# Performance work log

Measured on AMD Instinct MI355X. Metric: run time of the kernel, lower is better.

## Reference

```python
import jax, jax.numpy as jnp
import numpy as np

V = 1_000_000   # variables
F = 4_200_000   # functions (clauses), ratio ~4.2
K = 3           # literals per clause
E = K * F       # edges
T = 5           # fixed number of peel iterations (peel update is idempotent once converged)


def setup_inputs() -> dict:
    key = jax.random.key(0)
    k1, k2 = jax.random.split(key, 2)
    vidx = jax.random.randint(k1, (E,), 0, V, dtype=jnp.int32)
    fidx = jnp.repeat(jnp.arange(F, dtype=jnp.int32), K)  # each clause touches K variables
    graph_map = jnp.stack([vidx, fidx])  # [2, E]
    edge_feature = (2 * jax.random.randint(k2, (E,), 0, 2) - 1).astype(jnp.float32)  # +/-1 literal signs
    active_variables = jnp.ones((V, 1), jnp.float32)
    active_functions = jnp.ones((F, 1), jnp.float32)
    return dict(graph_map=graph_map, edge_feature=edge_feature,
                active_variables=active_variables, active_functions=active_functions)


def reference(graph_map, edge_feature, active_variables, active_functions):
    """Peeling propagation over the bipartite variable-function graph.

    Equivalent to the torch sparse-mm formulation:
      vf_map @ x        == segment_sum(x[fidx], vidx, V)
      signed_vf_map @ x == segment_sum(edge_feature * x[fidx], vidx, V)
      vf_map^T @ y      == segment_sum(y[vidx], fidx, F)
    """
    nV = active_variables.shape[0]
    nF = active_functions.shape[0]
    vidx = graph_map[0]
    fidx = graph_map[1]
    ef = edge_feature[:, None]  # [E,1]

    def seg_v(x_f):        # vf_map @ x_f : [F,1] -> [V,1]
        return jax.ops.segment_sum(x_f[fidx], vidx, num_segments=nV)

    def seg_v_signed(x_f):  # signed_vf_map @ x_f
        return jax.ops.segment_sum(ef * x_f[fidx], vidx, num_segments=nV)

    def seg_f(x_v):        # vf_map^T @ x_v : [V,1] -> [F,1]
        return jax.ops.segment_sum(x_v[vidx], fidx, num_segments=nF)

    variable_degree = seg_v(active_functions)
    signed_variable_degree = seg_v_signed(active_functions)

    def step(carry, _):
        av, af, deg, sdeg = carry
        # variables whose active clause occurrences all share one sign
        single_v = (deg == jnp.abs(sdeg)).astype(deg.dtype) * av
        # active clauses touched by those variables become satisfied
        single_f = (seg_f(single_v) > 0).astype(af.dtype) * af
        deg = deg - seg_v(single_f) * av
        sdeg = sdeg - seg_v_signed(single_f) * av
        av = av * (1.0 - single_v)
        af = af * (1.0 - single_f)
        return (av, af, deg, sdeg), None

    (av, af, deg, sdeg), _ = jax.lax.scan(
        step, (active_variables, active_functions, variable_degree, signed_variable_degree),
        None, length=T)
    return deg  # residual variable degrees after peeling [V,1]
```

## Files before the change

kernel.cpp:

```cpp
#include <hip/hip_runtime.h>


static constexpr int Vn = 1000000;
static constexpr int Fn = 4200000;
static constexpr int Tn = 5;

static constexpr int SBLK = 2048;
static constexpr int FPB  = 2052;
static constexpr int BIN_BITS = 10;
static constexpr int BIN_SIZE = 1 << BIN_BITS;
static constexpr int NB  = (Vn + BIN_SIZE - 1) >> BIN_BITS;
static constexpr int NBP = 1024;
static constexpr int CH_BITS = 12;
static constexpr int CH_SIZE = 1 << CH_BITS;
static constexpr int NCH = (Vn + CH_SIZE - 1) >> CH_BITS;
static constexpr int RCAP = 3 * FPB;
static constexpr int RSTRIDE = (RCAP + 63) & ~63;
static constexpr int OROW = 1024;
static constexpr int AVW = NCH * (CH_SIZE / 64);

__global__ __launch_bounds__(256) void k_pack_sort(
    const int* __restrict__ vidx, const float* __restrict__ ef,
    const float* __restrict__ afunc,
    unsigned long long* __restrict__ gpack,
    unsigned short* __restrict__ offs,
    unsigned short* __restrict__ sorted,
    unsigned int* __restrict__ tmp,
    unsigned char* __restrict__ tgrp)
{
    __shared__ unsigned int hist[NBP];
    __shared__ unsigned int cur[NBP];
    __shared__ unsigned int wsum[4];
    __shared__ unsigned int s_total;
    __shared__ __align__(16) unsigned short st[RSTRIDE];

    const int k = blockIdx.x;
    const int f0 = k * FPB;
    int n = Fn - f0; if (n < 0) n = 0; if (n > FPB) n = FPB;
    const int n4 = n >> 2;

    for (int i = threadIdx.x; i < NBP; i += 256) hist[i] = 0u;
    __syncthreads();

    for (int j = threadIdx.x; j < n4; j += 256) {
        const int fb = f0 + 4 * j, e = 3 * fb;
        int4 va = *(const int4*)(vidx + e);
        int4 vb = *(const int4*)(vidx + e + 4);
        int4 vc = *(const int4*)(vidx + e + 8);
        float4 ea = *(const float4*)(ef + e);
        float4 eb = *(const float4*)(ef + e + 4);
        float4 ec = *(const float4*)(ef + e + 8);
        float4 a4 = *(const float4*)(afunc + fb);
        int      vv[12] = {va.x, va.y, va.z, va.w, vb.x, vb.y, vb.z, vb.w, vc.x, vc.y, vc.z, vc.w};
        float    ss[12] = {ea.x, ea.y, ea.z, ea.w, eb.x, eb.y, eb.z, eb.w, ec.x, ec.y, ec.z, ec.w};
        float    aa[4]  = {a4.x, a4.y, a4.z, a4.w};
        unsigned long long gq[4];
        #pragma unroll
        for (int q = 0; q < 4; ++q) {
            int v0 = vv[3 * q], v1 = vv[3 * q + 1], v2 = vv[3 * q + 2];
            unsigned int s0 = ss[3 * q]     > 0.0f ? 1u : 0u;
            unsigned int s1 = ss[3 * q + 1] > 0.0f ? 1u : 0u;
            unsigned int s2 = ss[3 * q + 2] > 0.0f ? 1u : 0u;
            unsigned int act = aa[q] != 0.0f ? 1u : 0u;
            gq[q] = (unsigned long long)(unsigned int)v0
                  | ((unsigned long long)(unsigned int)v1 << 20)
                  | ((unsigned long long)(unsigned int)v2 << 40)
                  | ((unsigned long long)s0 << 60)
                  | ((unsigned long long)s1 << 61)
                  | ((unsigned long long)s2 << 62)
                  | ((unsigned long long)act << 63);
            if (act) {
                atomicAdd(&hist[v0 >> BIN_BITS], 1u);
                atomicAdd(&hist[v1 >> BIN_BITS], 1u);
                atomicAdd(&hist[v2 >> BIN_BITS], 1u);
            }
        }
        *(ulonglong2*)(gpack + fb)     = make_ulonglong2(gq[0], gq[1]);
        *(ulonglong2*)(gpack + fb + 2) = make_ulonglong2(gq[2], gq[3]);
    }
    for (int i = 4 * n4 + threadIdx.x; i < n; i += 256) {
        const int f = f0 + i, e0 = 3 * f;
        int v0 = vidx[e0], v1 = vidx[e0 + 1], v2 = vidx[e0 + 2];
        unsigned int s0 = ef[e0]     > 0.0f ? 1u : 0u;
        unsigned int s1 = ef[e0 + 1] > 0.0f ? 1u : 0u;
        unsigned int s2 = ef[e0 + 2] > 0.0f ? 1u : 0u;
        unsigned int act = afunc[f] != 0.0f ? 1u : 0u;
        unsigned long long g = (unsigned long long)(unsigned int)v0
                             | ((unsigned long long)(unsigned int)v1 << 20)
                             | ((unsigned long long)(unsigned int)v2 << 40)
                             | ((unsigned long long)s0 << 60)
                             | ((unsigned long long)s1 << 61)
                             | ((unsigned long long)s2 << 62)
                             | ((unsigned long long)act << 63);
        gpack[f] = g;
        if (act) {
            atomicAdd(&hist[v0 >> BIN_BITS], 1u);
            atomicAdd(&hist[v1 >> BIN_BITS], 1u);
            atomicAdd(&hist[v2 >> BIN_BITS], 1u);
        }
    }
    __syncthreads();

    {
        const int t = threadIdx.x, lane = t & 63, wid = t >> 6;
        unsigned int a0 = hist[4 * t], a1 = hist[4 * t + 1];
        unsigned int a2 = hist[4 * t + 2], a3 = hist[4 * t + 3];
        unsigned int tsum = a0 + a1 + a2 + a3;
        unsigned int x = tsum;
        #pragma unroll
        for (int off = 1; off < 64; off <<= 1) {
            unsigned int y = (unsigned int)__shfl_up((int)x, off);
            if (lane >= off) x += y;
        }
        if (lane == 63) wsum[wid] = x;
        __syncthreads();
        unsigned int wbase = 0;
        for (int w = 0; w < wid; ++w) wbase += wsum[w];
        unsigned int e0x = wbase + x - tsum;
        unsigned int e1x = e0x + a0, e2x = e1x + a1, e3x = e2x + a2;
        cur[4 * t] = e0x; cur[4 * t + 1] = e1x; cur[4 * t + 2] = e2x; cur[4 * t + 3] = e3x;
        if (t == 255) s_total = e3x + a3;
        unsigned short* row = offs + (size_t)k * OROW;
        if (4 * t     <= NB) row[4 * t]     = (unsigned short)e0x;
        if (4 * t + 1 <= NB) row[4 * t + 1] = (unsigned short)e1x;
        if (4 * t + 2 <= NB) row[4 * t + 2] = (unsigned short)e2x;
        if (4 * t + 3 <= NB) row[4 * t + 3] = (unsigned short)e3x;
    }
    __syncthreads();

    for (int j = threadIdx.x; j < n4; j += 256) {
        const int fb = f0 + 4 * j;
        ulonglong2 ga = *(const ulonglong2*)(gpack + fb);
        ulonglong2 gb = *(const ulonglong2*)(gpack + fb + 2);
        unsigned long long gq[4] = {ga.x, ga.y, gb.x, gb.y};
        #pragma unroll
        for (int q = 0; q < 4; ++q) {
            unsigned long long g = gq[q];
            if ((long long)g < 0) {
                unsigned int v0 = (unsigned int)(g & 0xFFFFFu);
                unsigned int v1 = (unsigned int)((g >> 20) & 0xFFFFFu);
                unsigned int v2 = (unsigned int)((g >> 40) & 0xFFFFFu);
                unsigned int sl0 = atomicAdd(&cur[v0 >> BIN_BITS], 1u);
                st[sl0] = (unsigned short)((v0 & (CH_SIZE - 1)) | ((unsigned int)((g >> 60) & 1u) << CH_BITS));
                unsigned int sl1 = atomicAdd(&cur[v1 >> BIN_BITS], 1u);
                st[sl1] = (unsigned short)((v1 & (CH_SIZE - 1)) | ((unsigned int)((g >> 61) & 1u) << CH_BITS));
                unsigned int sl2 = atomicAdd(&cur[v2 >> BIN_BITS], 1u);
                st[sl2] = (unsigned short)((v2 & (CH_SIZE - 1)) | ((unsigned int)((g >> 62) & 1u) << CH_BITS));
            }
        }
    }
    for (int i = 4 * n4 + threadIdx.x; i < n; i += 256) {
        unsigned long long g = gpack[f0 + i];
        if ((long long)g < 0) {
            unsigned int v0 = (unsigned int)(g & 0xFFFFFu);
            unsigned int v1 = (unsigned int)((g >> 20) & 0xFFFFFu);
            unsigned int v2 = (unsigned int)((g >> 40) & 0xFFFFFu);
            unsigned int sl0 = atomicAdd(&cur[v0 >> BIN_BITS], 1u);
            st[sl0] = (unsigned short)((v0 & (CH_SIZE - 1)) | ((unsigned int)((g >> 60) & 1u) << CH_BITS));
            unsigned int sl1 = atomicAdd(&cur[v1 >> BIN_BITS], 1u);
            st[sl1] = (unsigned short)((v1 & (CH_SIZE - 1)) | ((unsigned int)((g >> 61) & 1u) << CH_BITS));
            unsigned int sl2 = atomicAdd(&cur[v2 >> BIN_BITS], 1u);
            st[sl2] = (unsigned short)((v2 & (CH_SIZE - 1)) | ((unsigned int)((g >> 62) & 1u) << CH_BITS));
        }
    }
    __syncthreads();

    {
        const int tot = (int)s_total;
        const int nvec = (tot + 7) >> 3;
        int4* __restrict__ dst = (int4*)(sorted + (size_t)k * RSTRIDE);
        const int4* __restrict__ src = (const int4*)st;
        for (int i = threadIdx.x; i < nvec; i += 256) dst[i] = src[i];
    }

    {
        const int gt = blockIdx.x * 256 + threadIdx.x;
        const int gs = SBLK * 256;
        for (int i = gt; i < Vn; i += gs) tmp[i] = 0u;
        for (int i = gt; i < AVW; i += gs) tgrp[i] = 0;
    }
}

__global__ __launch_bounds__(256) void k_transpose(const unsigned short* __restrict__ in,
                                                   unsigned short* __restrict__ out) {
    __shared__ unsigned short t[64][65];
    const int bx = blockIdx.x;
    const int by = blockIdx.y;
    for (int i = threadIdx.x; i < 64 * 64; i += 256) {
        int r = i >> 6, c = i & 63;
        t[r][c] = in[(size_t)(by * 64 + r) * OROW + (bx * 64 + c)];
    }
    __syncthreads();
    for (int i = threadIdx.x; i < 64 * 64; i += 256) {
        int r = i >> 6, c = i & 63;
        out[(size_t)(bx * 64 + r) * SBLK + (by * 64 + c)] = t[c][r];
    }
}

__device__ __forceinline__ unsigned char subdirty8(unsigned long long m) {
    unsigned char b = 0;
    #pragma unroll
    for (int j = 0; j < 8; ++j) b |= (unsigned char)((((m >> (8 * j)) & 0xFFull) ? 1u : 0u) << j);
    return b;
}

__global__ __launch_bounds__(1024) void k_accum(
    const unsigned short* __restrict__ offs_T,
    const unsigned short* __restrict__ sorted,
    const float* __restrict__ avars,
    unsigned int* __restrict__ packed,
    unsigned long long* __restrict__ avm,
    unsigned long long* __restrict__ svm,
    unsigned char* __restrict__ sgrp8)
{
    __shared__ unsigned int acc[CH_SIZE];
    __shared__ unsigned short row0[SBLK];
    __shared__ unsigned short row1[SBLK];
    const int c = blockIdx.x;
    const int r0 = 4 * c;
    const int r1 = (4 * c + 4 < NB) ? (4 * c + 4) : NB;
    for (int i = threadIdx.x; i < CH_SIZE; i += 1024) acc[i] = 0u;
    for (int i = threadIdx.x; i < SBLK; i += 1024) {
        row0[i] = offs_T[(size_t)r0 * SBLK + i];
        row1[i] = offs_T[(size_t)r1 * SBLK + i];
    }
    __syncthreads();
    for (int k = threadIdx.x; k < SBLK; k += 1024) {
        const int s0 = row0[k], s1 = row1[k];
        const unsigned short* seg = sorted + (size_t)k * RSTRIDE;
        int e = s0;
        for (; e < s1 && (e & 3); ++e) {
            unsigned int p = seg[e];
            atomicAdd(&acc[p & (CH_SIZE - 1)], 0x10000u | (p >> CH_BITS));
        }
        for (; e + 4 <= s1; e += 4) {
            unsigned long long q = *(const unsigned long long*)(seg + e);
            #pragma unroll
            for (int j = 0; j < 4; ++j) {
                unsigned int p = (unsigned int)((q >> (16 * j)) & 0xFFFFu);
                atomicAdd(&acc[p & (CH_SIZE - 1)], 0x10000u | (p >> CH_BITS));
            }
        }
        for (; e < s1; ++e) {
            unsigned int p = seg[e];
            atomicAdd(&acc[p & (CH_SIZE - 1)], 0x10000u | (p >> CH_BITS));
        }
    }
    __syncthreads();
    const int vbase = c << CH_BITS;
    for (int i = threadIdx.x; i < CH_SIZE; i += 1024) {
        int v = vbase + i;
        bool valid = v < Vn;
        unsigned int p = valid ? acc[i] : 0u;
        bool av = valid && (avars[v] != 0.0f);
        unsigned int cnt = p >> 16, pos = p & 0xFFFFu;
        bool sv = av && (pos == 0u || pos == cnt);
        unsigned long long avb = __ballot(av);
        unsigned long long svb = __ballot(sv);
        if (valid) packed[v] = p;
        if ((threadIdx.x & 63) == 0) {
            avm[v >> 6] = avb;
            svm[v >> 6] = svb;
            sgrp8[v >> 6] = subdirty8(svb);
        }
    }
}

__device__ __forceinline__ void fire_one(unsigned long long g, int f,
                                         unsigned long long* __restrict__ gpack,
                                         const unsigned int* __restrict__ svm32,
                                         const unsigned char* __restrict__ s8,
                                         unsigned int* __restrict__ tmp,
                                         unsigned char* __restrict__ tgrp)
{
    if ((long long)g >= 0) return;
    unsigned int v0 = (unsigned int)(g & 0xFFFFFu);
    unsigned int v1 = (unsigned int)((g >> 20) & 0xFFFFFu);
    unsigned int v2 = (unsigned int)((g >> 40) & 0xFFFFFu);
    unsigned int h0 = (unsigned int)(s8[v0 >> 6] >> ((v0 >> 3) & 7u)) & 1u;
    unsigned int h1 = (unsigned int)(s8[v1 >> 6] >> ((v1 >> 3) & 7u)) & 1u;
    unsigned int h2 = (unsigned int)(s8[v2 >> 6] >> ((v2 >> 3) & 7u)) & 1u;
    if (!(h0 | h1 | h2)) return;
    unsigned int hit = ((svm32[v0 >> 5] >> (v0 & 31u)) |
                        (svm32[v1 >> 5] >> (v1 & 31u)) |
                        (svm32[v2 >> 5] >> (v2 & 31u))) & 1u;
    if (!hit) return;
    gpack[f] = g & ~(1ull << 63);
    atomicAdd(&tmp[v0], 0x10000u | (unsigned int)((g >> 60) & 1u));
    atomicAdd(&tmp[v1], 0x10000u | (unsigned int)((g >> 61) & 1u));
    atomicAdd(&tmp[v2], 0x10000u | (unsigned int)((g >> 62) & 1u));
    tgrp[v0 >> 6] = 1; tgrp[v1 >> 6] = 1; tgrp[v2 >> 6] = 1;
}

__global__ __launch_bounds__(256) void k_funcs(unsigned long long* __restrict__ gpack,
                        const unsigned int* __restrict__ svm32,
                        const unsigned char* __restrict__ sgrp8,
                        unsigned int* __restrict__ tmp,
                        unsigned char* __restrict__ tgrp)
{
    __shared__ __align__(16) unsigned char s8[AVW];
    for (int i = threadIdx.x; i < AVW / 16; i += 256)
        ((int4*)s8)[i] = ((const int4*)sgrp8)[i];
    __syncthreads();
    const int gid = blockIdx.x * 256 + threadIdx.x;
    const int f = 8 * gid;
    if (f >= Fn) return;
    ulonglong2 ga = *(const ulonglong2*)(gpack + f);
    ulonglong2 gb = *(const ulonglong2*)(gpack + f + 2);
    ulonglong2 gc = *(const ulonglong2*)(gpack + f + 4);
    ulonglong2 gd = *(const ulonglong2*)(gpack + f + 6);
    fire_one(ga.x, f,     gpack, svm32, s8, tmp, tgrp);
    fire_one(ga.y, f + 1, gpack, svm32, s8, tmp, tgrp);
    fire_one(gb.x, f + 2, gpack, svm32, s8, tmp, tgrp);
    fire_one(gb.y, f + 3, gpack, svm32, s8, tmp, tgrp);
    fire_one(gc.x, f + 4, gpack, svm32, s8, tmp, tgrp);
    fire_one(gc.y, f + 5, gpack, svm32, s8, tmp, tgrp);
    fire_one(gd.x, f + 6, gpack, svm32, s8, tmp, tgrp);
    fire_one(gd.y, f + 7, gpack, svm32, s8, tmp, tgrp);
}

__global__ void k_update(unsigned int* __restrict__ packed,
                         unsigned int* __restrict__ tmp,
                         unsigned long long* __restrict__ avm,
                         unsigned long long* __restrict__ svm,
                         unsigned char* __restrict__ sgrp8,
                         unsigned char* __restrict__ tgrp,
                         float* __restrict__ deg, int write_deg)
{
    const int v = blockIdx.x * blockDim.x + threadIdx.x;
    const int lane = threadIdx.x & 63;
    const bool valid = v < Vn;
    unsigned long long avw = 0ull, svw = 0ull;
    unsigned char tg = 0;
    if (valid) {
        avw = avm[v >> 6]; svw = svm[v >> 6];
        tg = tgrp[v >> 6];
    }
    if (!write_deg && !tg && svw == 0ull) return;
    const bool av_old = valid && ((avw >> lane) & 1ull);
    const bool sv     = valid && ((svw >> lane) & 1ull);
    const bool av_new = av_old && !sv;
    unsigned int p = 0u;
    if (valid) {
        p = packed[v];
        if (tg) {
            unsigned int tp = tmp[v];
            if (tp != 0u) {
                if (av_old) { p -= tp; packed[v] = p; }
                tmp[v] = 0u;
            }
        }
    }
    const unsigned int c = p >> 16, pos = p & 0xFFFFu;
    const bool nsv = av_new && (pos == 0u || pos == c);
    unsigned long long nsvb = __ballot(nsv);
    if (lane == 0 && valid) {
        svm[v >> 6] = nsvb;
        avm[v >> 6] = avw & ~svw;
        sgrp8[v >> 6] = subdirty8(nsvb);
        if (tg) tgrp[v >> 6] = 0;
    }
    if (write_deg && valid) deg[v] = (float)c;
}

extern "C" void kernel_launch(void* const* d_in, const int* in_sizes, int n_in,
                              void* d_out, int out_size, void* d_ws, size_t ws_size,
                              hipStream_t stream) {
    const int*   graph_map        = (const int*)d_in[0];
    const float* edge_feature     = (const float*)d_in[1];
    const float* active_variables = (const float*)d_in[2];
    const float* active_functions = (const float*)d_in[3];
    const int* vidx = graph_map;

    float* deg = (float*)d_out;
    char* ws = (char*)d_ws;
    size_t off = 0;
    auto alloc = [&](size_t bytes) -> void* {
        void* p = ws + off; off += (bytes + 255) & ~(size_t)255; return p;
    };
    unsigned long long* gpack = (unsigned long long*)alloc(8ull * Fn);
    unsigned int* packed      = (unsigned int*)alloc(4ull * Vn);
    unsigned long long* avm   = (unsigned long long*)alloc(8ull * AVW);
    unsigned long long* svm   = (unsigned long long*)alloc(8ull * AVW);
    unsigned char* sgrp8      = (unsigned char*)alloc(AVW);
    unsigned char* tgrp       = (unsigned char*)alloc(AVW);
    unsigned short* offs      = (unsigned short*)alloc(2ull * SBLK * OROW);
    unsigned short* offs_T    = (unsigned short*)alloc(2ull * SBLK * OROW);
    unsigned short* sorted    = (unsigned short*)alloc(2ull * SBLK * RSTRIDE);
    unsigned int* tmp         = (unsigned int*)alloc(4ull * Vn);

    const int BS = 256;
    const int gV = (Vn + BS - 1) / BS;
    const int gF8 = (Fn / 8 + BS - 1) / BS;

    k_pack_sort<<<SBLK, 256, 0, stream>>>(vidx, edge_feature, active_functions,
                                          gpack, offs, sorted, tmp, tgrp);
    k_transpose<<<dim3(OROW / 64, SBLK / 64), 256, 0, stream>>>(offs, offs_T);
    k_accum<<<NCH, 1024, 0, stream>>>(offs_T, sorted, active_variables, packed, avm, svm, sgrp8);
    for (int t = 0; t < Tn; ++t) {
        k_funcs<<<gF8, BS, 0, stream>>>(gpack, (const unsigned int*)svm, sgrp8, tmp, tgrp);
        k_update<<<gV, BS, 0, stream>>>(packed, tmp, avm, svm, sgrp8, tgrp, deg, (t == Tn - 1) ? 1 : 0);
    }
}
```

Baseline: 312.3 us.

## Replace binned sort-based degree accumulation with direct global atomics and persistent funcs grid

Drops the per-block histogram/counting-sort, offset transpose and chunked shared-memory accumulation kernels. Degrees and signed counts are now accumulated with global atomicAdd directly into the packed per-variable word during packing, followed by a simple decode kernel. A separate zeroing kernel is added, and k_funcs becomes a grid-stride loop over a fixed 1024 blocks so the per-block shared sgrp8 load is amortized. This trades the sort's locality for about 12.6M scattered global atomics onto 1M addresses.

```diff
diff --git a/kernel.cpp b/kernel.cpp
--- a/kernel.cpp
+++ b/kernel.cpp
@@ -5,196 +5,66 @@
 static constexpr int Fn = 4200000;
 static constexpr int Tn = 5;
 
-static constexpr int SBLK = 2048;
-static constexpr int FPB  = 2052;
-static constexpr int BIN_BITS = 10;
-static constexpr int BIN_SIZE = 1 << BIN_BITS;
-static constexpr int NB  = (Vn + BIN_SIZE - 1) >> BIN_BITS;
-static constexpr int NBP = 1024;
-static constexpr int CH_BITS = 12;
-static constexpr int CH_SIZE = 1 << CH_BITS;
-static constexpr int NCH = (Vn + CH_SIZE - 1) >> CH_BITS;
-static constexpr int RCAP = 3 * FPB;
-static constexpr int RSTRIDE = (RCAP + 63) & ~63;
-static constexpr int OROW = 1024;
+static constexpr int CH_SIZE = 4096;
+static constexpr int NCH = (Vn + CH_SIZE - 1) / CH_SIZE;
 static constexpr int AVW = NCH * (CH_SIZE / 64);
 
-__global__ __launch_bounds__(256) void k_pack_sort(
+__global__ __launch_bounds__(256) void k_zero(unsigned int* __restrict__ packed,
+                                              unsigned int* __restrict__ tmp,
+                                              unsigned char* __restrict__ tgrp)
+{
+    const int i = blockIdx.x * 256 + threadIdx.x;
+    const int4 z = make_int4(0, 0, 0, 0);
+    if (i < Vn / 4) {
+        ((int4*)packed)[i] = z;
+        ((int4*)tmp)[i] = z;
+    }
+    if (i < AVW / 16) ((int4*)tgrp)[i] = z;
+}
+
+__global__ __launch_bounds__(256) void k_pack(
     const int* __restrict__ vidx, const float* __restrict__ ef,
     const float* __restrict__ afunc,
     unsigned long long* __restrict__ gpack,
-    unsigned short* __restrict__ offs,
-    unsigned short* __restrict__ sorted,
-    unsigned int* __restrict__ tmp,
-    unsigned char* __restrict__ tgrp)
-{
-    __shared__ unsigned int hist[NBP];
-    __shared__ unsigned int cur[NBP];
-    __shared__ unsigned int wsum[4];
-    __shared__ unsigned int s_total;
-    __shared__ __align__(16) unsigned short st[RSTRIDE];
-
-    const int k = blockIdx.x;
-    const int f0 = k * FPB;
-    int n = Fn - f0; if (n < 0) n = 0; if (n > FPB) n = FPB;
-    const int n4 = n >> 2;
-
-    for (int i = threadIdx.x; i < NBP; i += 256) hist[i] = 0u;
-    __syncthreads();
-
-    for (int j = threadIdx.x; j < n4; j += 256) {
-        const int fb = f0 + 4 * j, e = 3 * fb;
-        int4 va = *(const int4*)(vidx + e);
-        int4 vb = *(const int4*)(vidx + e + 4);
-        int4 vc = *(const int4*)(vidx + e + 8);
-        float4 ea = *(const float4*)(ef + e);
-        float4 eb = *(const float4*)(ef + e + 4);
-        float4 ec = *(const float4*)(ef + e + 8);
-        float4 a4 = *(const float4*)(afunc + fb);
-        int      vv[12] = {va.x, va.y, va.z, va.w, vb.x, vb.y, vb.z, vb.w, vc.x, vc.y, vc.z, vc.w};
-        float    ss[12] = {ea.x, ea.y, ea.z, ea.w, eb.x, eb.y, eb.z, eb.w, ec.x, ec.y, ec.z, ec.w};
-        float    aa[4]  = {a4.x, a4.y, a4.z, a4.w};
-        unsigned long long gq[4];
-        #pragma unroll
-        for (int q = 0; q < 4; ++q) {
-            int v0 = vv[3 * q], v1 = vv[3 * q + 1], v2 = vv[3 * q + 2];
-            unsigned int s0 = ss[3 * q]     > 0.0f ? 1u : 0u;
-            unsigned int s1 = ss[3 * q + 1] > 0.0f ? 1u : 0u;
-            unsigned int s2 = ss[3 * q + 2] > 0.0f ? 1u : 0u;
-            unsigned int act = aa[q] != 0.0f ? 1u : 0u;
-            gq[q] = (unsigned long long)(unsigned int)v0
-                  | ((unsigned long long)(unsigned int)v1 << 20)
-                  | ((unsigned long long)(unsigned int)v2 << 40)
-                  | ((unsigned long long)s0 << 60)
-                  | ((unsigned long long)s1 << 61)
-                  | ((unsigned long long)s2 << 62)
-                  | ((unsigned long long)act << 63);
-            if (act) {
-                atomicAdd(&hist[v0 >> BIN_BITS], 1u);
-                atomicAdd(&hist[v1 >> BIN_BITS], 1u);
-                atomicAdd(&hist[v2 >> BIN_BITS], 1u);
-            }
+    unsigned int* __restrict__ packed)
+{
+    const int gid = blockIdx.x * 256 + threadIdx.x;
+    const int f = 4 * gid;
+    if (f >= Fn) return;
+    const int e = 3 * f;
+    int4 va = *(const int4*)(vidx + e);
+    int4 vb = *(const int4*)(vidx + e + 4);
+    int4 vc = *(const int4*)(vidx + e + 8);
+    float4 ea = *(const float4*)(ef + e);
+    float4 eb = *(const float4*)(ef + e + 4);
+    float4 ec = *(const float4*)(ef + e + 8);
+    float4 a4 = *(const float4*)(afunc + f);
+    int      vv[12] = {va.x, va.y, va.z, va.w, vb.x, vb.y, vb.z, vb.w, vc.x, vc.y, vc.z, vc.w};
+    float    ss[12] = {ea.x, ea.y, ea.z, ea.w, eb.x, eb.y, eb.z, eb.w, ec.x, ec.y, ec.z, ec.w};
+    float    aa[4]  = {a4.x, a4.y, a4.z, a4.w};
+    unsigned long long gq[4];
+    #pragma unroll
+    for (int q = 0; q < 4; ++q) {
+        int v0 = vv[3 * q], v1 = vv[3 * q + 1], v2 = vv[3 * q + 2];
+        unsigned int s0 = ss[3 * q]     > 0.0f ? 1u : 0u;
+        unsigned int s1 = ss[3 * q + 1] > 0.0f ? 1u : 0u;
+        unsigned int s2 = ss[3 * q + 2] > 0.0f ? 1u : 0u;
+        unsigned int act = aa[q] != 0.0f ? 1u : 0u;
+        gq[q] = (unsigned long long)(unsigned int)v0
+              | ((unsigned long long)(unsigned int)v1 << 20)
+              | ((unsigned long long)(unsigned int)v2 << 40)
+              | ((unsigned long long)s0 << 60)
+              | ((unsigned long long)s1 << 61)
+              | ((unsigned long long)s2 << 62)
+              | ((unsigned long long)act << 63);
+        if (act) {
+            atomicAdd(&packed[v0], 0x10000u | s0);
+            atomicAdd(&packed[v1], 0x10000u | s1);
+            atomicAdd(&packed[v2], 0x10000u | s2);
         }
-        *(ulonglong2*)(gpack + fb)     = make_ulonglong2(gq[0], gq[1]);
-        *(ulonglong2*)(gpack + fb + 2) = make_ulonglong2(gq[2], gq[3]);
-    }
-    for (int i = 4 * n4 + threadIdx.x; i < n; i += 256) {
-        const int f = f0 + i, e0 = 3 * f;
-        int v0 = vidx[e0], v1 = vidx[e0 + 1], v2 = vidx[e0 + 2];
-        unsigned int s0 = ef[e0]     > 0.0f ? 1u : 0u;
-        unsigned int s1 = ef[e0 + 1] > 0.0f ? 1u : 0u;
-        unsigned int s2 = ef[e0 + 2] > 0.0f ? 1u : 0u;
-        unsigned int act = afunc[f] != 0.0f ? 1u : 0u;
-        unsigned long long g = (unsigned long long)(unsigned int)v0
-                             | ((unsigned long long)(unsigned int)v1 << 20)
-                             | ((unsigned long long)(unsigned int)v2 << 40)
-                             | ((unsigned long long)s0 << 60)
-                             | ((unsigned long long)s1 << 61)
-                             | ((unsigned long long)s2 << 62)
-                             | ((unsigned long long)act << 63);
-        gpack[f] = g;
-        if (act) {
-            atomicAdd(&hist[v0 >> BIN_BITS], 1u);
-            atomicAdd(&hist[v1 >> BIN_BITS], 1u);
-            atomicAdd(&hist[v2 >> BIN_BITS], 1u);
-        }
-    }
-    __syncthreads();
-
-    {
-        const int t = threadIdx.x, lane = t & 63, wid = t >> 6;
-        unsigned int a0 = hist[4 * t], a1 = hist[4 * t + 1];
-        unsigned int a2 = hist[4 * t + 2], a3 = hist[4 * t + 3];
-        unsigned int tsum = a0 + a1 + a2 + a3;
-        unsigned int x = tsum;
-        #pragma unroll
-        for (int off = 1; off < 64; off <<= 1) {
-            unsigned int y = (unsigned int)__shfl_up((int)x, off);
-            if (lane >= off) x += y;
-        }
-        if (lane == 63) wsum[wid] = x;
-        __syncthreads();
-        unsigned int wbase = 0;
-        for (int w = 0; w < wid; ++w) wbase += wsum[w];
-        unsigned int e0x = wbase + x - tsum;
-        unsigned int e1x = e0x + a0, e2x = e1x + a1, e3x = e2x + a2;
-        cur[4 * t] = e0x; cur[4 * t + 1] = e1x; cur[4 * t + 2] = e2x; cur[4 * t + 3] = e3x;
-        if (t == 255) s_total = e3x + a3;
-        unsigned short* row = offs + (size_t)k * OROW;
-        if (4 * t     <= NB) row[4 * t]     = (unsigned short)e0x;
-        if (4 * t + 1 <= NB) row[4 * t + 1] = (unsigned short)e1x;
-        if (4 * t + 2 <= NB) row[4 * t + 2] = (unsigned short)e2x;
-        if (4 * t + 3 <= NB) row[4 * t + 3] = (unsigned short)e3x;
-    }
-    __syncthreads();
-
-    for (int j = threadIdx.x; j < n4; j += 256) {
-        const int fb = f0 + 4 * j;
-        ulonglong2 ga = *(const ulonglong2*)(gpack + fb);
-        ulonglong2 gb = *(const ulonglong2*)(gpack + fb + 2);
-        unsigned long long gq[4] = {ga.x, ga.y, gb.x, gb.y};
-        #pragma unroll
-        for (int q = 0; q < 4; ++q) {
-            unsigned long long g = gq[q];
-            if ((long long)g < 0) {
-                unsigned int v0 = (unsigned int)(g & 0xFFFFFu);
-                unsigned int v1 = (unsigned int)((g >> 20) & 0xFFFFFu);
-                unsigned int v2 = (unsigned int)((g >> 40) & 0xFFFFFu);
-                unsigned int sl0 = atomicAdd(&cur[v0 >> BIN_BITS], 1u);
-                st[sl0] = (unsigned short)((v0 & (CH_SIZE - 1)) | ((unsigned int)((g >> 60) & 1u) << CH_BITS));
-                unsigned int sl1 = atomicAdd(&cur[v1 >> BIN_BITS], 1u);
-                st[sl1] = (unsigned short)((v1 & (CH_SIZE - 1)) | ((unsigned int)((g >> 61) & 1u) << CH_BITS));
-                unsigned int sl2 = atomicAdd(&cur[v2 >> BIN_BITS], 1u);
-                st[sl2] = (unsigned short)((v2 & (CH_SIZE - 1)) | ((unsigned int)((g >> 62) & 1u) << CH_BITS));
-            }
-        }
-    }
-    for (int i = 4 * n4 + threadIdx.x; i < n; i += 256) {
-        unsigned long long g = gpack[f0 + i];
-        if ((long long)g < 0) {
-            unsigned int v0 = (unsigned int)(g & 0xFFFFFu);
-            unsigned int v1 = (unsigned int)((g >> 20) & 0xFFFFFu);
-            unsigned int v2 = (unsigned int)((g >> 40) & 0xFFFFFu);
-            unsigned int sl0 = atomicAdd(&cur[v0 >> BIN_BITS], 1u);
-            st[sl0] = (unsigned short)((v0 & (CH_SIZE - 1)) | ((unsigned int)((g >> 60) & 1u) << CH_BITS));
-            unsigned int sl1 = atomicAdd(&cur[v1 >> BIN_BITS], 1u);
-            st[sl1] = (unsigned short)((v1 & (CH_SIZE - 1)) | ((unsigned int)((g >> 61) & 1u) << CH_BITS));
-            unsigned int sl2 = atomicAdd(&cur[v2 >> BIN_BITS], 1u);
-            st[sl2] = (unsigned short)((v2 & (CH_SIZE - 1)) | ((unsigned int)((g >> 62) & 1u) << CH_BITS));
-        }
-    }
-    __syncthreads();
-
-    {
-        const int tot = (int)s_total;
-        const int nvec = (tot + 7) >> 3;
-        int4* __restrict__ dst = (int4*)(sorted + (size_t)k * RSTRIDE);
-        const int4* __restrict__ src = (const int4*)st;
-        for (int i = threadIdx.x; i < nvec; i += 256) dst[i] = src[i];
-    }
-
-    {
-        const int gt = blockIdx.x * 256 + threadIdx.x;
-        const int gs = SBLK * 256;
-        for (int i = gt; i < Vn; i += gs) tmp[i] = 0u;
-        for (int i = gt; i < AVW; i += gs) tgrp[i] = 0;
-    }
-}
-
-__global__ __launch_bounds__(256) void k_transpose(const unsigned short* __restrict__ in,
-                                                   unsigned short* __restrict__ out) {
-    __shared__ unsigned short t[64][65];
-    const int bx = blockIdx.x;
-    const int by = blockIdx.y;
-    for (int i = threadIdx.x; i < 64 * 64; i += 256) {
-        int r = i >> 6, c = i & 63;
-        t[r][c] = in[(size_t)(by * 64 + r) * OROW + (bx * 64 + c)];
-    }
-    __syncthreads();
-    for (int i = threadIdx.x; i < 64 * 64; i += 256) {
-        int r = i >> 6, c = i & 63;
-        out[(size_t)(bx * 64 + r) * SBLK + (by * 64 + c)] = t[c][r];
-    }
+    }
+    *(ulonglong2*)(gpack + f)     = make_ulonglong2(gq[0], gq[1]);
+    *(ulonglong2*)(gpack + f + 2) = make_ulonglong2(gq[2], gq[3]);
 }
 
 __device__ __forceinline__ unsigned char subdirty8(unsigned long long m) {
@@ -204,65 +74,26 @@
     return b;
 }
 
-__global__ __launch_bounds__(1024) void k_accum(
-    const unsigned short* __restrict__ offs_T,
-    const unsigned short* __restrict__ sorted,
+__global__ __launch_bounds__(256) void k_decode(
+    const unsigned int* __restrict__ packed,
     const float* __restrict__ avars,
-    unsigned int* __restrict__ packed,
     unsigned long long* __restrict__ avm,
     unsigned long long* __restrict__ svm,
     unsigned char* __restrict__ sgrp8)
 {
-    __shared__ unsigned int acc[CH_SIZE];
-    __shared__ unsigned short row0[SBLK];
-    __shared__ unsigned short row1[SBLK];
-    const int c = blockIdx.x;
-    const int r0 = 4 * c;
-    const int r1 = (4 * c + 4 < NB) ? (4 * c + 4) : NB;
-    for (int i = threadIdx.x; i < CH_SIZE; i += 1024) acc[i] = 0u;
-    for (int i = threadIdx.x; i < SBLK; i += 1024) {
-        row0[i] = offs_T[(size_t)r0 * SBLK + i];
-        row1[i] = offs_T[(size_t)r1 * SBLK + i];
-    }
-    __syncthreads();
-    for (int k = threadIdx.x; k < SBLK; k += 1024) {
-        const int s0 = row0[k], s1 = row1[k];
-        const unsigned short* seg = sorted + (size_t)k * RSTRIDE;
-        int e = s0;
-        for (; e < s1 && (e & 3); ++e) {
-            unsigned int p = seg[e];
-            atomicAdd(&acc[p & (CH_SIZE - 1)], 0x10000u | (p >> CH_BITS));
-        }
-        for (; e + 4 <= s1; e += 4) {
-            unsigned long long q = *(const unsigned long long*)(seg + e);
-            #pragma unroll
-            for (int j = 0; j < 4; ++j) {
-                unsigned int p = (unsigned int)((q >> (16 * j)) & 0xFFFFu);
-                atomicAdd(&acc[p & (CH_SIZE - 1)], 0x10000u | (p >> CH_BITS));
-            }
-        }
-        for (; e < s1; ++e) {
-            unsigned int p = seg[e];
-            atomicAdd(&acc[p & (CH_SIZE - 1)], 0x10000u | (p >> CH_BITS));
-        }
-    }
-    __syncthreads();
-    const int vbase = c << CH_BITS;
-    for (int i = threadIdx.x; i < CH_SIZE; i += 1024) {
-        int v = vbase + i;
-        bool valid = v < Vn;
-        unsigned int p = valid ? acc[i] : 0u;
-        bool av = valid && (avars[v] != 0.0f);
-        unsigned int cnt = p >> 16, pos = p & 0xFFFFu;
-        bool sv = av && (pos == 0u || pos == cnt);
-        unsigned long long avb = __ballot(av);
-        unsigned long long svb = __ballot(sv);
-        if (valid) packed[v] = p;
-        if ((threadIdx.x & 63) == 0) {
-            avm[v >> 6] = avb;
-            svm[v >> 6] = svb;
-            sgrp8[v >> 6] = subdirty8(svb);
-        }
+    const int v = blockIdx.x * 256 + threadIdx.x;
+    const int lane = threadIdx.x & 63;
+    const bool valid = v < Vn;
+    unsigned int p = valid ? packed[v] : 0u;
+    bool av = valid && (avars[v] != 0.0f);
+    unsigned int cnt = p >> 16, pos = p & 0xFFFFu;
+    bool sv = av && (pos == 0u || pos == cnt);
+    unsigned long long avb = __ballot(av);
+    unsigned long long svb = __ballot(sv);
+    if (lane == 0 && (v >> 6) < AVW) {
+        avm[v >> 6] = avb;
+        svm[v >> 6] = svb;
+        sgrp8[v >> 6] = subdirty8(svb);
     }
 }
 
@@ -292,6 +123,8 @@
     tgrp[v0 >> 6] = 1; tgrp[v1 >> 6] = 1; tgrp[v2 >> 6] = 1;
 }
 
+static constexpr int FBLOCKS = 1024;
+
 __global__ __launch_bounds__(256) void k_funcs(unsigned long long* __restrict__ gpack,
                         const unsigned int* __restrict__ svm32,
                         const unsigned char* __restrict__ sgrp8,
@@ -302,21 +135,21 @@
     for (int i = threadIdx.x; i < AVW / 16; i += 256)
         ((int4*)s8)[i] = ((const int4*)sgrp8)[i];
     __syncthreads();
-    const int gid = blockIdx.x * 256 + threadIdx.x;
-    const int f = 8 * gid;
-    if (f >= Fn) return;
-    ulonglong2 ga = *(const ulonglong2*)(gpack + f);
-    ulonglong2 gb = *(const ulonglong2*)(gpack + f + 2);
-    ulonglong2 gc = *(const ulonglong2*)(gpack + f + 4);
-    ulonglong2 gd = *(const ulonglong2*)(gpack + f + 6);
-    fire_one(ga.x, f,     gpack, svm32, s8, tmp, tgrp);
-    fire_one(ga.y, f + 1, gpack, svm32, s8, tmp, tgrp);
-    fire_one(gb.x, f + 2, gpack, svm32, s8, tmp, tgrp);
-    fire_one(gb.y, f + 3, gpack, svm32, s8, tmp, tgrp);
-    fire_one(gc.x, f + 4, gpack, svm32, s8, tmp, tgrp);
-    fire_one(gc.y, f + 5, gpack, svm32, s8, tmp, tgrp);
-    fire_one(gd.x, f + 6, gpack, svm32, s8, tmp, tgrp);
-    fire_one(gd.y, f + 7, gpack, svm32, s8, tmp, tgrp);
+    const int nthr = FBLOCKS * 256;
+    for (int f = (blockIdx.x * 256 + threadIdx.x) * 8; f < Fn; f += nthr * 8) {
+        ulonglong2 ga = *(const ulonglong2*)(gpack + f);
+        ulonglong2 gb = *(const ulonglong2*)(gpack + f + 2);
+        ulonglong2 gc = *(const ulonglong2*)(gpack + f + 4);
+        ulonglong2 gd = *(const ulonglong2*)(gpack + f + 6);
+        fire_one(ga.x, f,     gpack, svm32, s8, tmp, tgrp);
+        fire_one(ga.y, f + 1, gpack, svm32, s8, tmp, tgrp);
+        fire_one(gb.x, f + 2, gpack, svm32, s8, tmp, tgrp);
+        fire_one(gb.y, f + 3, gpack, svm32, s8, tmp, tgrp);
+        fire_one(gc.x, f + 4, gpack, svm32, s8, tmp, tgrp);
+        fire_one(gc.y, f + 5, gpack, svm32, s8, tmp, tgrp);
+        fire_one(gd.x, f + 6, gpack, svm32, s8, tmp, tgrp);
+        fire_one(gd.y, f + 7, gpack, svm32, s8, tmp, tgrp);
+    }
 }
 
 __global__ void k_update(unsigned int* __restrict__ packed,
@@ -380,25 +213,22 @@
     };
     unsigned long long* gpack = (unsigned long long*)alloc(8ull * Fn);
     unsigned int* packed      = (unsigned int*)alloc(4ull * Vn);
+    unsigned int* tmp         = (unsigned int*)alloc(4ull * Vn);
     unsigned long long* avm   = (unsigned long long*)alloc(8ull * AVW);
     unsigned long long* svm   = (unsigned long long*)alloc(8ull * AVW);
     unsigned char* sgrp8      = (unsigned char*)alloc(AVW);
     unsigned char* tgrp       = (unsigned char*)alloc(AVW);
-    unsigned short* offs      = (unsigned short*)alloc(2ull * SBLK * OROW);
-    unsigned short* offs_T    = (unsigned short*)alloc(2ull * SBLK * OROW);
-    unsigned short* sorted    = (unsigned short*)alloc(2ull * SBLK * RSTRIDE);
-    unsigned int* tmp         = (unsigned int*)alloc(4ull * Vn);
 
     const int BS = 256;
     const int gV = (Vn + BS - 1) / BS;
-    const int gF8 = (Fn / 8 + BS - 1) / BS;
-
-    k_pack_sort<<<SBLK, 256, 0, stream>>>(vidx, edge_feature, active_functions,
-                                          gpack, offs, sorted, tmp, tgrp);
-    k_transpose<<<dim3(OROW / 64, SBLK / 64), 256, 0, stream>>>(offs, offs_T);
-    k_accum<<<NCH, 1024, 0, stream>>>(offs_T, sorted, active_variables, packed, avm, svm, sgrp8);
+    const int gZ = (Vn / 4 + BS - 1) / BS;
+    const int gP = (Fn / 4 + BS - 1) / BS;
+
+    k_zero<<<gZ, BS, 0, stream>>>(packed, tmp, tgrp);
+    k_pack<<<gP, BS, 0, stream>>>(vidx, edge_feature, active_functions, gpack, packed);
+    k_decode<<<gV, BS, 0, stream>>>(packed, active_variables, avm, svm, sgrp8);
     for (int t = 0; t < Tn; ++t) {
-        k_funcs<<<gF8, BS, 0, stream>>>(gpack, (const unsigned int*)svm, sgrp8, tmp, tgrp);
+        k_funcs<<<FBLOCKS, BS, 0, stream>>>(gpack, (const unsigned int*)svm, sgrp8, tmp, tgrp);
         k_update<<<gV, BS, 0, stream>>>(packed, tmp, avm, svm, sgrp8, tgrp, deg, (t == Tn - 1) ? 1 : 0);
     }
 }
```

Result: slower. 694.4 us (+122.3%).
